# Kernel tuning notes

Measured on AMD Instinct MI355X. Metric: run time of the kernel, lower is better.

The kernel has to match this reference:

```python
import jax, jax.numpy as jnp
import numpy as np

N_NODES = 50000

def setup_inputs() -> dict:
    key = jax.random.key(0)
    k1, k2, k3, k4, k5 = jax.random.split(key, 5)
    x = jax.random.normal(k1, (4, N_NODES, 128), dtype=jnp.float32)
    weights = jax.random.normal(k2, (128, 64), dtype=jnp.float32) * (np.sqrt(2.0) * np.sqrt(6.0 / (128 + 64)))
    edge_vals = jax.random.uniform(k3, (800000,), dtype=jnp.float32)
    edge_rows = jax.random.randint(k4, (800000,), 0, N_NODES, dtype=jnp.int32)
    edge_cols = jax.random.randint(k5, (800000,), 0, N_NODES, dtype=jnp.int32)
    return {"x": x, "weights": weights, "edge_vals": edge_vals,
            "edge_rows": edge_rows, "edge_cols": edge_cols}

def reference(x, weights, edge_vals, edge_rows, edge_cols):
    # x: [B, N, Din]; weights: [Din, Dout]; adj as COO edges (shared across batch)
    pre = jnp.einsum('bni,io->bno', x, weights)          # dense GEMM per sample
    msg = pre[:, edge_cols, :] * edge_vals[None, :, None]  # [B, E, Dout] gather+scale
    # sparse adj @ pre: scatter-add messages to destination rows, per batch sample
    agg = jax.vmap(lambda m: jax.ops.segment_sum(m, edge_rows, num_segments=N_NODES))(msg)
    return jax.nn.relu(agg)
```

## Files before the change

### kernel.cpp

```cpp
#include <hip/hip_runtime.h>
#include <hip/hip_bf16.h>


#define B_BATCH 4
#define DIN 128
#define DOUT 64
#define CAP 64

typedef float f32x4 __attribute__((ext_vector_type(4)));
typedef short s16x8 __attribute__((ext_vector_type(8)));

static __device__ __forceinline__ unsigned short f2bf(float f) {
  unsigned u = __builtin_bit_cast(unsigned, f);
  unsigned r = (u + 0x7fff + ((u >> 16) & 1)) >> 16;
  return (unsigned short)r;
}
static __device__ __forceinline__ float lo16(unsigned u) {
  return __builtin_bit_cast(float, u << 16);
}
static __device__ __forceinline__ float hi16(unsigned u) {
  return __builtin_bit_cast(float, u & 0xffff0000u);
}

__global__ __launch_bounds__(256) void prep_wfrag_zero_kernel(
    const float* __restrict__ w, uint4* __restrict__ wimg,
    int* __restrict__ cnt, int n) {
  const int t = threadIdx.x;
  if (blockIdx.x != 0) {
    int i = (blockIdx.x - 1) * 256 + t;
    if (i < n) cnt[i] = 0;
    return;
  }
  for (int i = 0; i < 8; ++i) {
    int idx = i * 256 + t;
    int fslot = idx >> 6;
    int lane = idx & 63;
    int term = fslot & 1;
    int cks = fslot >> 1;
    int ct = cks >> 2, ks = cks & 3;
    int nn = ct * 16 + (lane & 15);
    int kb = ks * 32 + 4 * ((lane >> 4) & 3);
    unsigned short e[8];
#pragma unroll
    for (int j = 0; j < 8; ++j) {
      int k = kb + 16 * (j >> 2) + (j & 3);
      float wv = w[k * DOUT + nn];
      unsigned ub = __builtin_bit_cast(unsigned, wv);
      unsigned hib = ub & 0xffff0000u;
      if (term == 0) {
        e[j] = (unsigned short)(hib >> 16);
      } else {
        float lof = wv - __builtin_bit_cast(float, hib);
        e[j] = (unsigned short)(__builtin_bit_cast(unsigned, lof) >> 16);
      }
    }
    uint4 q;
    q.x = (unsigned)e[0] | ((unsigned)e[1] << 16);
    q.y = (unsigned)e[2] | ((unsigned)e[3] << 16);
    q.z = (unsigned)e[4] | ((unsigned)e[5] << 16);
    q.w = (unsigned)e[6] | ((unsigned)e[7] << 16);
    wimg[idx] = q;
  }
}

__global__ __launch_bounds__(256) void gemm_fill_kernel(
    const float* __restrict__ x, const uint4* __restrict__ wimg,
    unsigned short* __restrict__ pre16, int N, int nWaveTiles,
    const int* __restrict__ erows, const int* __restrict__ ecols,
    const float* __restrict__ evals, int* __restrict__ cnt,
    int2* __restrict__ epk, int nE) {
  __shared__ uint4 wlds[2048];
  const int t = threadIdx.x;
  for (int i = t; i < 2048; i += 256) wlds[i] = wimg[i];
  __syncthreads();

  const int wtile = blockIdx.x * 4 + (t >> 6);
  if (wtile < nWaveTiles) {
    const int lane = t & 63;
    const int rowg = (lane >> 4) & 3;
    const int rloc = lane & 15;

    f32x4 acc[2][4];
#pragma unroll
    for (int rs = 0; rs < 2; ++rs)
#pragma unroll
      for (int ct = 0; ct < 4; ++ct) acc[rs][ct] = (f32x4){0.f, 0.f, 0.f, 0.f};

    const float* xb = x + (size_t)wtile * 32 * DIN;

#pragma unroll
    for (int ks = 0; ks < 4; ++ks) {
      s16x8 Ah[2], Al[2];
#pragma unroll
      for (int rs = 0; rs < 2; ++rs) {
        const float* xp = xb + (rs * 16 + rloc) * DIN + ks * 32 + 4 * rowg;
        float4 a0 = *(const float4*)xp;
        float4 a1 = *(const float4*)(xp + 16);

        unsigned b0 = __builtin_bit_cast(unsigned, a0.x);
        unsigned b1 = __builtin_bit_cast(unsigned, a0.y);
        unsigned b2 = __builtin_bit_cast(unsigned, a0.z);
        unsigned b3 = __builtin_bit_cast(unsigned, a0.w);
        unsigned c0 = __builtin_bit_cast(unsigned, a1.x);
        unsigned c1 = __builtin_bit_cast(unsigned, a1.y);
        unsigned c2 = __builtin_bit_cast(unsigned, a1.z);
        unsigned c3 = __builtin_bit_cast(unsigned, a1.w);

        union { s16x8 v; unsigned u[4]; } H, L;
        H.u[0] = (b0 >> 16) | (b1 & 0xffff0000u);
        H.u[1] = (b2 >> 16) | (b3 & 0xffff0000u);
        H.u[2] = (c0 >> 16) | (c1 & 0xffff0000u);
        H.u[3] = (c2 >> 16) | (c3 & 0xffff0000u);

        float l0 = a0.x - hi16(b0);
        float l1 = a0.y - hi16(b1);
        float l2 = a0.z - hi16(b2);
        float l3 = a0.w - hi16(b3);
        float l4 = a1.x - hi16(c0);
        float l5 = a1.y - hi16(c1);
        float l6 = a1.z - hi16(c2);
        float l7 = a1.w - hi16(c3);
        L.u[0] = (__builtin_bit_cast(unsigned, l0) >> 16) |
                 (__builtin_bit_cast(unsigned, l1) & 0xffff0000u);
        L.u[1] = (__builtin_bit_cast(unsigned, l2) >> 16) |
                 (__builtin_bit_cast(unsigned, l3) & 0xffff0000u);
        L.u[2] = (__builtin_bit_cast(unsigned, l4) >> 16) |
                 (__builtin_bit_cast(unsigned, l5) & 0xffff0000u);
        L.u[3] = (__builtin_bit_cast(unsigned, l6) >> 16) |
                 (__builtin_bit_cast(unsigned, l7) & 0xffff0000u);
        Ah[rs] = H.v;
        Al[rs] = L.v;
      }

#pragma unroll
      for (int ct = 0; ct < 4; ++ct) {
        const int fbase = (ct * 4 + ks) * 2;
        s16x8 Bh = *(const s16x8*)&wlds[fbase * 64 + lane];
        s16x8 Bl = *(const s16x8*)&wlds[(fbase + 1) * 64 + lane];
#pragma unroll
        for (int rs = 0; rs < 2; ++rs) {
          acc[rs][ct] = __builtin_amdgcn_mfma_f32_16x16x32_bf16(Ah[rs], Bh, acc[rs][ct], 0, 0, 0);
          acc[rs][ct] = __builtin_amdgcn_mfma_f32_16x16x32_bf16(Ah[rs], Bl, acc[rs][ct], 0, 0, 0);
          acc[rs][ct] = __builtin_amdgcn_mfma_f32_16x16x32_bf16(Al[rs], Bh, acc[rs][ct], 0, 0, 0);
        }
      }
    }

#pragma unroll
    for (int rs = 0; rs < 2; ++rs) {
#pragma unroll
      for (int r = 0; r < 4; ++r) {
        int m = wtile * 32 + rs * 16 + 4 * rowg + r;
        int b = m / N;
        int n = m - b * N;
        size_t o = (size_t)n * 256 + b * 64 + rloc;
#pragma unroll
        for (int ct = 0; ct < 4; ++ct) {
          pre16[o + ct * 16] = f2bf(acc[rs][ct][r]);
        }
      }
    }
  }

  const int stride = gridDim.x * 256;
  for (int e = blockIdx.x * 256 + t; e < nE; e += stride) {
    int r = erows[e];
    int slot = atomicAdd(&cnt[r], 1);
    if (slot < CAP)
      epk[r * CAP + slot] = make_int2(ecols[e], __builtin_bit_cast(int, evals[e]));
  }
}

__global__ __launch_bounds__(256) void gather_rows_kernel(
    const unsigned short* __restrict__ pre16, const int* __restrict__ cnt,
    const int2* __restrict__ epk, float* __restrict__ out, int N, int NS) {
  const int wid  = blockIdx.x * 4 + (threadIdx.x >> 6);
  const int lane = threadIdx.x & 63;
  if (wid >= N) return;

  const int m    = min(cnt[wid], CAP);
  const int eh   = lane >> 5;
  const int loff = ((lane >> 3) & 3) * 64 + (lane & 7) * 8;

  int   c = 0;
  float v = 0.0f;
  if (lane < m) {
    int2 r = epk[wid * CAP + lane];
    c = r.x;
    v = __builtin_bit_cast(float, r.y);
  }

  float a0 = 0.f, a1 = 0.f, a2 = 0.f, a3 = 0.f;
  float a4 = 0.f, a5 = 0.f, a6 = 0.f, a7 = 0.f;

  auto edge2 = [&](int j) {
    int   cj = __shfl(c, j + eh, 64);
    float vj = __shfl(v, j + eh, 64);
    const uint4 q = *(const uint4*)(pre16 + (size_t)cj * 256 + loff);
    a0 = fmaf(vj, lo16(q.x), a0);
    a1 = fmaf(vj, hi16(q.x), a1);
    a2 = fmaf(vj, lo16(q.y), a2);
    a3 = fmaf(vj, hi16(q.y), a3);
    a4 = fmaf(vj, lo16(q.z), a4);
    a5 = fmaf(vj, hi16(q.z), a5);
    a6 = fmaf(vj, lo16(q.w), a6);
    a7 = fmaf(vj, hi16(q.w), a7);
  };

  int j = 0;
  for (; j + 15 < m; j += 16) {
    edge2(j);      edge2(j + 2);  edge2(j + 4);  edge2(j + 6);
    edge2(j + 8);  edge2(j + 10); edge2(j + 12); edge2(j + 14);
  }
  for (; j + 7 < m; j += 8) { edge2(j); edge2(j + 2); edge2(j + 4); edge2(j + 6); }
  for (; j + 1 < m; j += 2) { edge2(j); }
  if (j < m) {
    int   cj = __shfl(c, j, 64);
    float vj = __shfl(v, j, 64);
    if (eh) vj = 0.0f;
    const uint4 q = *(const uint4*)(pre16 + (size_t)cj * 256 + loff);
    a0 = fmaf(vj, lo16(q.x), a0);
    a1 = fmaf(vj, hi16(q.x), a1);
    a2 = fmaf(vj, lo16(q.y), a2);
    a3 = fmaf(vj, hi16(q.y), a3);
    a4 = fmaf(vj, lo16(q.z), a4);
    a5 = fmaf(vj, hi16(q.z), a5);
    a6 = fmaf(vj, lo16(q.w), a6);
    a7 = fmaf(vj, hi16(q.w), a7);
  }

  a0 += __shfl_xor(a0, 32, 64);
  a1 += __shfl_xor(a1, 32, 64);
  a2 += __shfl_xor(a2, 32, 64);
  a3 += __shfl_xor(a3, 32, 64);
  a4 += __shfl_xor(a4, 32, 64);
  a5 += __shfl_xor(a5, 32, 64);
  a6 += __shfl_xor(a6, 32, 64);
  a7 += __shfl_xor(a7, 32, 64);

  if (lane < 32) {
    const int b   = lane >> 3;
    const int ch8 = (lane & 7) * 8;
    size_t o = (size_t)b * NS + (size_t)wid * DOUT + ch8;
    *(float4*)&out[o]     = make_float4(fmaxf(a0, 0.f), fmaxf(a1, 0.f),
                                        fmaxf(a2, 0.f), fmaxf(a3, 0.f));
    *(float4*)&out[o + 4] = make_float4(fmaxf(a4, 0.f), fmaxf(a5, 0.f),
                                        fmaxf(a6, 0.f), fmaxf(a7, 0.f));
  }
}

extern "C" void kernel_launch(void* const* d_in, const int* in_sizes, int n_in,
                              void* d_out, int out_size, void* d_ws, size_t ws_size,
                              hipStream_t stream) {
  const float* x     = (const float*)d_in[0];
  const float* w     = (const float*)d_in[1];
  const float* evals = (const float*)d_in[2];
  const int*   erows = (const int*)d_in[3];
  const int*   ecols = (const int*)d_in[4];
  float* out = (float*)d_out;

  const int N  = in_sizes[0] / (B_BATCH * DIN);
  const int E  = in_sizes[2];
  const int M  = B_BATCH * N;
  const int NS = N * DOUT;
  const int nWaveTiles = M / 32;

  size_t off = 0;
  auto alloc = [&](size_t bytes) {
    size_t o = off;
    off += (bytes + 255) & ~(size_t)255;
    return o;
  };
  size_t pre_off  = alloc((size_t)M * DOUT * 2);
  size_t wimg_off = alloc((size_t)2048 * 16);
  size_t cnt_off  = alloc((size_t)N * 4);
  size_t epk_off  = alloc((size_t)N * CAP * 8);
  (void)ws_size;

  char* ws = (char*)d_ws;
  unsigned short* pre16 = (unsigned short*)(ws + pre_off);
  uint4* wimg = (uint4*)(ws + wimg_off);
  int*   cnt  = (int*)(ws + cnt_off);
  int2*  epk  = (int2*)(ws + epk_off);

  prep_wfrag_zero_kernel<<<1 + (N + 255) / 256, 256, 0, stream>>>(w, wimg, cnt, N);

  gemm_fill_kernel<<<(nWaveTiles + 3) / 4, 256, 0, stream>>>(
      x, wimg, pre16, N, nWaveTiles, erows, ecols, evals, cnt, epk, E);

  gather_rows_kernel<<<(N + 3) / 4, 256, 0, stream>>>(pre16, cnt, epk, out, N, NS);
}
```

Before: 131.5 us.

## Drop LDS weight staging, prefetch all x tiles into registers upfront

Removes the per-block copy of the 32KB weight fragment image into shared memory and the barrier that follows it, and reads the B fragments straight from global memory (L1/L2 cached) inside each k-step. All eight float4 x loads per row-slab are issued at the start so the memory requests are in flight together, and launch bounds ask for 3 blocks per CU. The output index math is also simplified to use 16-row slabs, which avoids a per-row division. The trade is more register pressure and repeated global/L2 reads of the weights in place of LDS reads.

```diff
diff --git a/kernel.cpp b/kernel.cpp
--- a/kernel.cpp
+++ b/kernel.cpp
@@ -63,39 +63,51 @@
   }
 }
 
-__global__ __launch_bounds__(256) void gemm_fill_kernel(
+__global__ __launch_bounds__(256, 3) void gemm_fill_kernel(
     const float* __restrict__ x, const uint4* __restrict__ wimg,
-    unsigned short* __restrict__ pre16, int N, int nWaveTiles,
+    unsigned short* __restrict__ pre16, int NB16 , int nWaveTiles,
     const int* __restrict__ erows, const int* __restrict__ ecols,
     const float* __restrict__ evals, int* __restrict__ cnt,
     int2* __restrict__ epk, int nE) {
-  __shared__ uint4 wlds[2048];
   const int t = threadIdx.x;
-  for (int i = t; i < 2048; i += 256) wlds[i] = wimg[i];
-  __syncthreads();
-
   const int wtile = blockIdx.x * 4 + (t >> 6);
+
   if (wtile < nWaveTiles) {
     const int lane = t & 63;
     const int rowg = (lane >> 4) & 3;
     const int rloc = lane & 15;
 
+    const float* xp = x + (size_t)wtile * 32 * DIN + rloc * DIN + 4 * rowg;
+    float4 X[2][4][2];
+#pragma unroll
+    for (int rs = 0; rs < 2; ++rs)
+#pragma unroll
+      for (int ks = 0; ks < 4; ++ks) {
+        X[rs][ks][0] = *(const float4*)(xp + rs * 16 * DIN + ks * 32);
+        X[rs][ks][1] = *(const float4*)(xp + rs * 16 * DIN + ks * 32 + 16);
+      }
+
     f32x4 acc[2][4];
 #pragma unroll
     for (int rs = 0; rs < 2; ++rs)
 #pragma unroll
       for (int ct = 0; ct < 4; ++ct) acc[rs][ct] = (f32x4){0.f, 0.f, 0.f, 0.f};
 
-    const float* xb = x + (size_t)wtile * 32 * DIN;
-
 #pragma unroll
     for (int ks = 0; ks < 4; ++ks) {
+      s16x8 Bh[4], Bl[4];
+#pragma unroll
+      for (int ct = 0; ct < 4; ++ct) {
+        const int fbase = (ct * 4 + ks) * 2;
+        Bh[ct] = *(const s16x8*)&wimg[fbase * 64 + lane];
+        Bl[ct] = *(const s16x8*)&wimg[(fbase + 1) * 64 + lane];
+      }
+
       s16x8 Ah[2], Al[2];
 #pragma unroll
       for (int rs = 0; rs < 2; ++rs) {
-        const float* xp = xb + (rs * 16 + rloc) * DIN + ks * 32 + 4 * rowg;
-        float4 a0 = *(const float4*)xp;
-        float4 a1 = *(const float4*)(xp + 16);
+        float4 a0 = X[rs][ks][0];
+        float4 a1 = X[rs][ks][1];
 
         unsigned b0 = __builtin_bit_cast(unsigned, a0.x);
         unsigned b1 = __builtin_bit_cast(unsigned, a0.y);
@@ -134,26 +146,23 @@
 
 #pragma unroll
       for (int ct = 0; ct < 4; ++ct) {
-        const int fbase = (ct * 4 + ks) * 2;
-        s16x8 Bh = *(const s16x8*)&wlds[fbase * 64 + lane];
-        s16x8 Bl = *(const s16x8*)&wlds[(fbase + 1) * 64 + lane];
 #pragma unroll
         for (int rs = 0; rs < 2; ++rs) {
-          acc[rs][ct] = __builtin_amdgcn_mfma_f32_16x16x32_bf16(Ah[rs], Bh, acc[rs][ct], 0, 0, 0);
-          acc[rs][ct] = __builtin_amdgcn_mfma_f32_16x16x32_bf16(Ah[rs], Bl, acc[rs][ct], 0, 0, 0);
-          acc[rs][ct] = __builtin_amdgcn_mfma_f32_16x16x32_bf16(Al[rs], Bh, acc[rs][ct], 0, 0, 0);
+          acc[rs][ct] = __builtin_amdgcn_mfma_f32_16x16x32_bf16(Ah[rs], Bh[ct], acc[rs][ct], 0, 0, 0);
+          acc[rs][ct] = __builtin_amdgcn_mfma_f32_16x16x32_bf16(Ah[rs], Bl[ct], acc[rs][ct], 0, 0, 0);
+          acc[rs][ct] = __builtin_amdgcn_mfma_f32_16x16x32_bf16(Al[rs], Bh[ct], acc[rs][ct], 0, 0, 0);
         }
       }
     }
 
 #pragma unroll
     for (int rs = 0; rs < 2; ++rs) {
+      int s = wtile * 2 + rs;
+      int b = s / NB16;
+      int nb = (s - b * NB16) * 16 + 4 * rowg;
 #pragma unroll
       for (int r = 0; r < 4; ++r) {
-        int m = wtile * 32 + rs * 16 + 4 * rowg + r;
-        int b = m / N;
-        int n = m - b * N;
-        size_t o = (size_t)n * 256 + b * 64 + rloc;
+        size_t o = (size_t)(nb + r) * 256 + b * 64 + rloc;
 #pragma unroll
         for (int ct = 0; ct < 4; ++ct) {
           pre16[o + ct * 16] = f2bf(acc[rs][ct][r]);
@@ -264,6 +273,7 @@
   const int M  = B_BATCH * N;
   const int NS = N * DOUT;
   const int nWaveTiles = M / 32;
+  const int NB16 = N / 16;
 
   size_t off = 0;
   auto alloc = [&](size_t bytes) {
@@ -286,7 +296,7 @@
   prep_wfrag_zero_kernel<<<1 + (N + 255) / 256, 256, 0, stream>>>(w, wimg, cnt, N);
 
   gemm_fill_kernel<<<(nWaveTiles + 3) / 4, 256, 0, stream>>>(
-      x, wimg, pre16, N, nWaveTiles, erows, ecols, evals, cnt, epk, E);
+      x, wimg, pre16, NB16, nWaveTiles, erows, ecols, evals, cnt, epk, E);
 
   gather_rows_kernel<<<(N + 3) / 4, 256, 0, stream>>>(pre16, cnt, epk, out, N, NS);
 }
```

New measurement: 125.4 us. 1.05x faster.
